# Optimization experiments

Hardware: AMD Instinct MI355X
Metric: run time of the kernel (lower is better)

The kernel has to match this reference:

```python
import jax, jax.numpy as jnp
import numpy as np

CHEB_K = 3


def setup_inputs() -> dict:
    key = jax.random.key(0)
    ks = jax.random.split(key, 7)
    B, N, D, E = 32, 2048, 64, 10
    return {
        "x": jax.random.normal(ks[0], (B, N, D), jnp.float32),
        "state": jnp.zeros((B, N, D), jnp.float32),
        "node_embeddings": jax.random.normal(ks[1], (N, E), jnp.float32),
        "gate_w_pool": 0.1 * jax.random.normal(ks[2], (E, CHEB_K, D, 2 * D), jnp.float32),
        "gate_b_pool": 0.1 * jax.random.normal(ks[3], (E, 2 * D), jnp.float32),
        "update_w_pool": 0.1 * jax.random.normal(ks[4], (E, CHEB_K, 2 * D, D), jnp.float32),
        "update_b_pool": 0.1 * jax.random.normal(ks[5], (E, D), jnp.float32),
    }


def _avwgcn(x, node_emb, w_pool, b_pool):
    # Adaptive adjacency from node embeddings: softmax(relu(E E^T)) over rows.
    N = node_emb.shape[0]
    adj = jax.nn.softmax(jax.nn.relu(node_emb @ node_emb.T), axis=1)  # [N,N]
    cheb = [jnp.eye(N, dtype=x.dtype), adj]
    for _ in range(2, CHEB_K):
        cheb.append(2.0 * adj @ cheb[-1] - cheb[-2])
    supports = jnp.stack(cheb, axis=0)  # [K,N,N]
    # Node-specific weights/bias from pools.
    weights = jnp.einsum('ne,ekio->nkio', node_emb, w_pool)  # [N,K,Ci,Co]
    bias = node_emb @ b_pool                                  # [N,Co]
    x_g = jnp.einsum('knm,bmi->bnki', supports, x)            # [B,N,K,Ci]
    return jnp.einsum('bnki,nkio->bno', x_g, weights) + bias  # [B,N,Co]


def reference(x, state, node_embeddings, gate_w_pool, gate_b_pool, update_w_pool, update_b_pool):
    # TGCRNCell.forward (note: `state` is ignored by the original forward;
    # input_and_state = x). dim_in == dim_out == hidden_dim.
    hidden_dim = x.shape[-1]
    z_r = jax.nn.sigmoid(_avwgcn(x, node_embeddings, gate_w_pool, gate_b_pool))
    z, r = z_r[..., :hidden_dim], z_r[..., hidden_dim:]
    candidate = jnp.concatenate([x, z], axis=-1)
    hc = jnp.tanh(_avwgcn(candidate, node_embeddings, update_w_pool, update_b_pool))
    h = r * x + (1.0 - r) * hc
    return h
```

## Files before the change

### kernel.cpp

```cpp
#include <hip/hip_runtime.h>

typedef _Float16 f16_t;
typedef float f32x4 __attribute__((ext_vector_type(4)));
typedef _Float16 f16x8 __attribute__((ext_vector_type(8)));

#define AS1 __attribute__((address_space(1)))
#define AS3 __attribute__((address_space(3)))

__device__ __forceinline__ void gload_lds16(const void* g, void* l) {
  __builtin_amdgcn_global_load_lds((const AS1 void*)g, (AS3 void*)l, 16, 0, 0);
}

__global__ __launch_bounds__(256) void adj_softmax(const float* __restrict__ emb,
                                                   f16_t* __restrict__ adjF) {
  __shared__ float vals[2048];
  __shared__ float red[16];
  const int n = blockIdx.x;
  const int t = threadIdx.x;
  const int lane = t & 63, wave = t >> 6;
  float en[10];
#pragma unroll
  for (int e = 0; e < 10; ++e) en[e] = emb[n * 10 + e];
  float lm = 0.0f;
  for (int m = t; m < 2048; m += 256) {
    const float* em = emb + m * 10;
    float d = 0.f;
#pragma unroll
    for (int e = 0; e < 10; ++e) d += en[e] * em[e];
    d = fmaxf(d, 0.0f);
    vals[m] = d;
    lm = fmaxf(lm, d);
  }
#pragma unroll
  for (int off = 32; off > 0; off >>= 1) lm = fmaxf(lm, __shfl_down(lm, off));
  if (lane == 0) red[wave] = lm;
  __syncthreads();
  const float gmax = fmaxf(fmaxf(red[0], red[1]), fmaxf(red[2], red[3]));
  float ls = 0.f;
  for (int m = t; m < 2048; m += 256) {
    float ev = expf(vals[m] - gmax);
    vals[m] = ev;
    ls += ev;
  }
#pragma unroll
  for (int off = 32; off > 0; off >>= 1) ls += __shfl_down(ls, off);
  if (lane == 0) red[8 + wave] = ls;
  __syncthreads();
  const float inv = 4096.0f / (red[8] + red[9] + red[10] + red[11]);
  for (int m = t; m < 2048; m += 256) {
    adjF[(long)n * 2048 + m] = (f16_t)(vals[m] * inv);
  }
}

__global__ __launch_bounds__(256) void split_xt(const float* __restrict__ x,
                                                f16_t* __restrict__ XTh) {
  __shared__ float tile[64][65];
  const int m0 = blockIdx.x * 64;
  const int b = blockIdx.y;
  const int tx = threadIdx.x & 63, ty = threadIdx.x >> 6;
  for (int r = ty; r < 64; r += 4)
    tile[r][tx] = x[(long)b * 131072 + (long)(m0 + r) * 64 + tx];
  __syncthreads();
  for (int r = ty; r < 64; r += 4) {
    long idx = (long)(b * 64 + r) * 2048 + m0 + tx;
    XTh[idx] = (f16_t)tile[tx][r];
  }
}

__global__ __launch_bounds__(256) void tsplit(const float* __restrict__ in,
                                              f16_t* __restrict__ oH, int R, int C) {
  __shared__ float tile[64][65];
  const int c0 = blockIdx.x * 64, r0 = blockIdx.y * 64;
  const int tx = threadIdx.x & 63, ty = threadIdx.x >> 6;
  for (int r = ty; r < 64; r += 4)
    tile[r][tx] = in[(long)(r0 + r) * C + c0 + tx];
  __syncthreads();
  for (int r = ty; r < 64; r += 4) {
    long idx = (long)(c0 + r) * R + r0 + tx;
    oH[idx] = (f16_t)tile[tx][r];
  }
}

__global__ __launch_bounds__(256) void permute_pool(const float* __restrict__ wp,
                                                    float* __restrict__ P,
                                                    int KI, int I, int O) {
  const int g = blockIdx.x * 256 + threadIdx.x;
  const int per = KI * O;
  const int e = g / per, rem = g % per;
  const int o = rem / KI, kk = rem % KI;
  const int k = kk / I, i = kk % I;
  P[g] = wp[(long)((e * 3 + k) * I + i) * O + o];
}

__global__ __launch_bounds__(256) void wgen(const float* __restrict__ P,
                                            const float* __restrict__ emb,
                                            f16_t* __restrict__ W) {
  __shared__ float es[160];
  const int c0 = blockIdx.x * 1024;
  const int n0 = blockIdx.y * 16;
  const int t = threadIdx.x;
  const int i4 = t * 4;
  if (t < 160) es[t] = emb[n0 * 10 + t];
  float4 p[10];
#pragma unroll
  for (int e = 0; e < 10; ++e)
    p[e] = *(const float4*)(P + (long)e * 24576 + c0 + i4);
  __syncthreads();
#pragma unroll 4
  for (int nn = 0; nn < 16; ++nn) {
    const float* ep = es + nn * 10;
    float v0 = 0.f, v1 = 0.f, v2 = 0.f, v3 = 0.f;
#pragma unroll
    for (int e = 0; e < 10; ++e) {
      const float ee = ep[e];
      v0 += ee * p[e].x; v1 += ee * p[e].y; v2 += ee * p[e].z; v3 += ee * p[e].w;
    }
    union { ushort4 u; f16_t h[4]; } o;
    o.h[0] = (f16_t)v0; o.h[1] = (f16_t)v1; o.h[2] = (f16_t)v2; o.h[3] = (f16_t)v3;
    *(ushort4*)(W + (long)(n0 + nn) * 24576 + c0 + i4) = o.u;
  }
}

template <int WT>
__global__ __launch_bounds__(256) void fgemm(const f16_t* __restrict__ A,
                                             const f16_t* __restrict__ B,
                                             float* __restrict__ Cf,
                                             f16_t* __restrict__ Th,
                                             int K, int ldc) {
  __shared__ __align__(16) f16_t Ash[128 * 64];
  __shared__ __align__(16) f16_t Bsh[64 * 64];
  const int t = threadIdx.x;
  const int wave = t >> 6, lane = t & 63;
  const long m0 = (long)blockIdx.y * 128;
  const long n0 = (long)blockIdx.x * 64;
  const int srow = t >> 3;
  const int sc8 = ((t & 7) ^ (srow & 7)) << 3;
  const int fr = lane & 15;
  const int quad = lane >> 4;
  const int wm = wave * 32;
  char* lA = (char*)Ash + wave * 1024;
  char* lB = (char*)Bsh + wave * 1024;
  f32x4 acc[2][4] = {};
  for (int k0 = 0; k0 < K; k0 += 64) {
#pragma unroll
    for (int q = 0; q < 4; ++q)
      gload_lds16(A + (m0 + q * 32 + srow) * K + k0 + sc8, lA + q * 4096);
#pragma unroll
    for (int q = 0; q < 2; ++q)
      gload_lds16(B + (n0 + q * 32 + srow) * K + k0 + sc8, lB + q * 4096);
    __syncthreads();
#pragma unroll
    for (int kh = 0; kh < 2; ++kh) {
      const int cbase = kh * 4 + quad;
      f16x8 ah[2], bh[4];
#pragma unroll
      for (int i = 0; i < 2; ++i) {
        const int r = wm + i * 16 + fr;
        ah[i] = *(const f16x8*)(Ash + r * 64 + ((cbase ^ (fr & 7)) << 3));
      }
#pragma unroll
      for (int j = 0; j < 4; ++j) {
        const int r = j * 16 + fr;
        bh[j] = *(const f16x8*)(Bsh + r * 64 + ((cbase ^ (fr & 7)) << 3));
      }
#pragma unroll
      for (int i = 0; i < 2; ++i)
#pragma unroll
        for (int j = 0; j < 4; ++j)
          acc[i][j] = __builtin_amdgcn_mfma_f32_16x16x32_f16(ah[i], bh[j], acc[i][j], 0, 0, 0);
    }
    __syncthreads();
  }
  const int crow = quad * 4, ccol = fr;
#pragma unroll
  for (int i = 0; i < 2; ++i)
#pragma unroll
    for (int j = 0; j < 4; ++j) {
      float v[4];
#pragma unroll
      for (int r = 0; r < 4; ++r) v[r] = acc[i][j][r] * 0.000244140625f;
      const long gmb = m0 + wm + i * 16 + crow;
      const long gn = n0 + j * 16 + ccol;
#pragma unroll
      for (int r = 0; r < 4; ++r) Cf[(gmb + r) * ldc + gn] = v[r];
      if (WT) {
        union { ushort4 u; f16_t h[4]; } ph;
#pragma unroll
        for (int r = 0; r < 4; ++r) ph.h[r] = (f16_t)v[r];
        *(ushort4*)(Th + gn * 2048 + gmb) = ph.u;
      }
    }
}

__global__ __launch_bounds__(256) void gate_kernel(
    const float* __restrict__ x, const float* __restrict__ Xg1f,
    const float* __restrict__ Xg2r, const f16_t* __restrict__ Wg,
    const float* __restrict__ bpool, const float* __restrict__ emb,
    float* __restrict__ Zf, f16_t* __restrict__ rb) {
  __shared__ __align__(16) f16_t Ahi[32 * 200];
  const int n = blockIdx.x;
  const int t = threadIdx.x;
  float en[10];
#pragma unroll
  for (int e = 0; e < 10; ++e) en[e] = emb[n * 10 + e];
  {
    const int b = t >> 3, i8 = (t & 7) * 8;
    const float* s0 = x + (long)b * 131072 + (long)n * 64 + i8;
    const float* s1 = Xg1f + (long)n * 2048 + b * 64 + i8;
    const float* s2 = Xg2r + (long)n * 2048 + b * 64 + i8;
    float v0[8], v1[8], v2[8];
#pragma unroll
    for (int j = 0; j < 8; ++j) v0[j] = s0[j];
#pragma unroll
    for (int j = 0; j < 8; ++j) v1[j] = s1[j];
#pragma unroll
    for (int j = 0; j < 8; ++j) v2[j] = 2.0f * s2[j] - v0[j];
    union { uint4 u; f16_t h[8]; } th;
#pragma unroll
    for (int j = 0; j < 8; ++j) th.h[j] = (f16_t)v0[j];
    *(uint4*)(Ahi + b * 200 + i8) = th.u;
#pragma unroll
    for (int j = 0; j < 8; ++j) th.h[j] = (f16_t)v1[j];
    *(uint4*)(Ahi + b * 200 + 64 + i8) = th.u;
#pragma unroll
    for (int j = 0; j < 8; ++j) th.h[j] = (f16_t)v2[j];
    *(uint4*)(Ahi + b * 200 + 128 + i8) = th.u;
  }
  __syncthreads();
  const int wave = t >> 6, lane = t & 63;
  const int ob = wave * 32;
  const int fr = lane & 15, qk = (lane >> 4) * 8;
  const f16_t* Wp0 = Wg + (long)n * 24576 + (ob + fr) * 192 + qk;
  const f16_t* Wp1 = Wp0 + 16 * 192;
  f32x4 acc[2][2] = {};
#pragma unroll
  for (int k0 = 0; k0 < 192; k0 += 32) {
    f16x8 b0 = *(const f16x8*)(Wp0 + k0);
    f16x8 b1 = *(const f16x8*)(Wp1 + k0);
    f16x8 a0 = *(const f16x8*)(Ahi + fr * 200 + k0 + qk);
    f16x8 a1 = *(const f16x8*)(Ahi + (16 + fr) * 200 + k0 + qk);
    acc[0][0] = __builtin_amdgcn_mfma_f32_16x16x32_f16(a0, b0, acc[0][0], 0, 0, 0);
    acc[1][0] = __builtin_amdgcn_mfma_f32_16x16x32_f16(a1, b0, acc[1][0], 0, 0, 0);
    acc[0][1] = __builtin_amdgcn_mfma_f32_16x16x32_f16(a0, b1, acc[0][1], 0, 0, 0);
    acc[1][1] = __builtin_amdgcn_mfma_f32_16x16x32_f16(a1, b1, acc[1][1], 0, 0, 0);
  }
  const int quad = lane >> 4;
#pragma unroll
  for (int j = 0; j < 2; ++j) {
    const int o = ob + j * 16 + fr;
    float bias = 0.f;
#pragma unroll
    for (int e = 0; e < 10; ++e) bias += en[e] * bpool[e * 128 + o];
#pragma unroll
    for (int i2 = 0; i2 < 2; ++i2)
#pragma unroll
      for (int r = 0; r < 4; ++r) {
        const int b = i2 * 16 + quad * 4 + r;
        float v = acc[i2][j][r] + bias;
        v = 1.0f / (1.0f + expf(-v));
        if (o < 64)
          Zf[(long)n * 2048 + b * 64 + o] = v;
        else
          rb[(long)n * 2048 + b * 64 + (o - 64)] = (f16_t)v;
      }
  }
}

__global__ __launch_bounds__(256) void update_kernel(
    const float* __restrict__ x, const float* __restrict__ Zf,
    const float* __restrict__ Xg1f, const float* __restrict__ Cgz1f,
    const float* __restrict__ Xg2r, const float* __restrict__ Cgz2r,
    const f16_t* __restrict__ Wu, const float* __restrict__ bpool,
    const float* __restrict__ emb, const f16_t* __restrict__ rb,
    float* __restrict__ out) {
  __shared__ __align__(16) f16_t Ahi[32 * 392];
  const int n = blockIdx.x;
  const int t = threadIdx.x;
  float en[10];
#pragma unroll
  for (int e = 0; e < 10; ++e) en[e] = emb[n * 10 + e];
#pragma unroll
  for (int r = 0; r < 2; ++r) {
    const int c = r * 2048 + t * 8;
    const int b = c >> 7, j = c & 127;
    const int lo64 = j & 63;
    const float* s0 = (j < 64) ? (x + (long)b * 131072 + (long)n * 64 + lo64)
                               : (Zf + (long)n * 2048 + b * 64 + lo64);
    const float* s1 = (j < 64) ? (Xg1f + (long)n * 2048 + b * 64 + lo64)
                               : (Cgz1f + (long)n * 2048 + b * 64 + lo64);
    const float* s2 = (j < 64) ? (Xg2r + (long)n * 2048 + b * 64 + lo64)
                               : (Cgz2r + (long)n * 2048 + b * 64 + lo64);
    float v0[8], v1[8], v2[8];
#pragma unroll
    for (int q = 0; q < 8; ++q) v0[q] = s0[q];
#pragma unroll
    for (int q = 0; q < 8; ++q) v1[q] = s1[q];
#pragma unroll
    for (int q = 0; q < 8; ++q) v2[q] = 2.0f * s2[q] - v0[q];
    union { uint4 u; f16_t h[8]; } th;
#pragma unroll
    for (int q = 0; q < 8; ++q) th.h[q] = (f16_t)v0[q];
    *(uint4*)(Ahi + b * 392 + j) = th.u;
#pragma unroll
    for (int q = 0; q < 8; ++q) th.h[q] = (f16_t)v1[q];
    *(uint4*)(Ahi + b * 392 + 128 + j) = th.u;
#pragma unroll
    for (int q = 0; q < 8; ++q) th.h[q] = (f16_t)v2[q];
    *(uint4*)(Ahi + b * 392 + 256 + j) = th.u;
  }
  __syncthreads();
  const int wave = t >> 6, lane = t & 63;
  const int ob = wave * 16;
  const int fr = lane & 15, qk = (lane >> 4) * 8;
  const f16_t* Wp = Wu + (long)n * 24576 + (ob + fr) * 384 + qk;
  f32x4 acc[2] = {};
#pragma unroll
  for (int k0 = 0; k0 < 384; k0 += 32) {
    f16x8 bhv = *(const f16x8*)(Wp + k0);
    f16x8 a0 = *(const f16x8*)(Ahi + fr * 392 + k0 + qk);
    f16x8 a1 = *(const f16x8*)(Ahi + (16 + fr) * 392 + k0 + qk);
    acc[0] = __builtin_amdgcn_mfma_f32_16x16x32_f16(a0, bhv, acc[0], 0, 0, 0);
    acc[1] = __builtin_amdgcn_mfma_f32_16x16x32_f16(a1, bhv, acc[1], 0, 0, 0);
  }
  const int quad = lane >> 4;
  const int og = ob + fr;
  float bias = 0.f;
#pragma unroll
  for (int e = 0; e < 10; ++e) bias += en[e] * bpool[e * 64 + og];
#pragma unroll
  for (int i2 = 0; i2 < 2; ++i2)
#pragma unroll
    for (int r = 0; r < 4; ++r) {
      const int b = i2 * 16 + quad * 4 + r;
      float hc = tanhf(acc[i2][r] + bias);
      float rr = (float)rb[(long)n * 2048 + b * 64 + og];
      float xv = x[(long)b * 131072 + (long)n * 64 + og];
      out[(long)b * 131072 + (long)n * 64 + og] = rr * xv + (1.0f - rr) * hc;
    }
}

extern "C" void kernel_launch(void* const* d_in, const int* in_sizes, int n_in,
                              void* d_out, int out_size, void* d_ws, size_t ws_size,
                              hipStream_t stream) {
  (void)in_sizes; (void)n_in; (void)out_size;
  const float* x   = (const float*)d_in[0];
  const float* emb = (const float*)d_in[2];
  const float* gwp = (const float*)d_in[3];
  const float* gbp = (const float*)d_in[4];
  const float* uwp = (const float*)d_in[5];
  const float* ubp = (const float*)d_in[6];
  float* out = (float*)d_out;
  char* ws = (char*)d_ws;

  if (ws_size < 194904064ull) return;

  float*  Xg1f  = (float*)(ws);
  float*  Xg2r  = (float*)(ws + 16777216);
  float*  Zf    = (float*)(ws + 33554432);
  f16_t*  T1h   = (f16_t*)(ws + 33554432);
  f16_t*  rb    = (f16_t*)(ws + 50331648);
  float*  Pg    = (float*)(ws + 58720256);
  float*  Pu    = (float*)(ws + 59703296);
  f16_t*  adjF  = (f16_t*)(ws + 60686336);
  f16_t*  Sh    = (f16_t*)(ws + 69074944);
  f16_t*  Wg    = (f16_t*)(ws + 85852160);
  f16_t*  T2h   = (f16_t*)(ws + 85852160);
  f16_t*  Wu    = (f16_t*)(ws + 60686336);
  float*  Cgz1f = (float*)(ws + 161349632);
  float*  Cgz2r = (float*)(ws + 178126848);

  permute_pool<<<960, 256, 0, stream>>>(gwp, Pg, 192, 64, 128);
  permute_pool<<<960, 256, 0, stream>>>(uwp, Pu, 384, 128, 64);
  wgen<<<dim3(24, 128), 256, 0, stream>>>(Pg, emb, Wg);
  adj_softmax<<<2048, 256, 0, stream>>>(emb, adjF);
  split_xt<<<dim3(32, 32), 256, 0, stream>>>(x, Sh);

  fgemm<1><<<dim3(32, 16), 256, 0, stream>>>(adjF, Sh, Xg1f, T1h, 2048, 2048);
  fgemm<0><<<dim3(32, 16), 256, 0, stream>>>(adjF, T1h, Xg2r, nullptr, 2048, 2048);

  gate_kernel<<<2048, 256, 0, stream>>>(x, Xg1f, Xg2r, Wg, gbp, emb, Zf, rb);

  tsplit<<<dim3(32, 32), 256, 0, stream>>>(Zf, Sh, 2048, 2048);
  fgemm<1><<<dim3(32, 16), 256, 0, stream>>>(adjF, Sh, Cgz1f, T2h, 2048, 2048);
  fgemm<0><<<dim3(32, 16), 256, 0, stream>>>(adjF, T2h, Cgz2r, nullptr, 2048, 2048);

  wgen<<<dim3(24, 128), 256, 0, stream>>>(Pu, emb, Wu);
  update_kernel<<<2048, 256, 0, stream>>>(x, Zf, Xg1f, Cgz1f, Xg2r, Cgz2r, Wu,
                                          ubp, emb, rb, out);
}
```

Measured before the change: 381.2 us.

## Store graph-conv intermediates in fp16 and widen weight generation stores

Intermediate buffers (Xg1, Xg2, Z, Cgz1, Cgz2) are written and read as fp16 instead of fp32. This halves memory traffic between the GEMMs, the gate/update kernels and tsplit, and shrinks the workspace layout to match. wgen now computes 8 outputs per thread and writes them with 128-bit nontemporal stores, so half as many blocks are launched. The risk is extra rounding error in the intermediates and the Chebyshev recombination.

```diff
diff --git a/kernel.cpp b/kernel.cpp
--- a/kernel.cpp
+++ b/kernel.cpp
@@ -3,6 +3,7 @@
 typedef _Float16 f16_t;
 typedef float f32x4 __attribute__((ext_vector_type(4)));
 typedef _Float16 f16x8 __attribute__((ext_vector_type(8)));
+typedef unsigned int u32x4 __attribute__((ext_vector_type(4)));
 
 #define AS1 __attribute__((address_space(1)))
 #define AS3 __attribute__((address_space(3)))
@@ -67,13 +68,13 @@
   }
 }
 
-__global__ __launch_bounds__(256) void tsplit(const float* __restrict__ in,
+__global__ __launch_bounds__(256) void tsplit(const f16_t* __restrict__ in,
                                               f16_t* __restrict__ oH, int R, int C) {
   __shared__ float tile[64][65];
   const int c0 = blockIdx.x * 64, r0 = blockIdx.y * 64;
   const int tx = threadIdx.x & 63, ty = threadIdx.x >> 6;
   for (int r = ty; r < 64; r += 4)
-    tile[r][tx] = in[(long)(r0 + r) * C + c0 + tx];
+    tile[r][tx] = (float)in[(long)(r0 + r) * C + c0 + tx];
   __syncthreads();
   for (int r = ty; r < 64; r += 4) {
     long idx = (long)(c0 + r) * R + r0 + tx;
@@ -96,35 +97,41 @@
                                             const float* __restrict__ emb,
                                             f16_t* __restrict__ W) {
   __shared__ float es[160];
-  const int c0 = blockIdx.x * 1024;
+  const int c0 = blockIdx.x * 2048;
   const int n0 = blockIdx.y * 16;
   const int t = threadIdx.x;
-  const int i4 = t * 4;
+  const int i8 = t * 8;
   if (t < 160) es[t] = emb[n0 * 10 + t];
-  float4 p[10];
-#pragma unroll
-  for (int e = 0; e < 10; ++e)
-    p[e] = *(const float4*)(P + (long)e * 24576 + c0 + i4);
-  __syncthreads();
-#pragma unroll 4
+  float4 pa[10], pb[10];
+#pragma unroll
+  for (int e = 0; e < 10; ++e) {
+    pa[e] = *(const float4*)(P + (long)e * 24576 + c0 + i8);
+    pb[e] = *(const float4*)(P + (long)e * 24576 + c0 + i8 + 4);
+  }
+  __syncthreads();
+#pragma unroll 2
   for (int nn = 0; nn < 16; ++nn) {
     const float* ep = es + nn * 10;
-    float v0 = 0.f, v1 = 0.f, v2 = 0.f, v3 = 0.f;
+    float v[8] = {0.f, 0.f, 0.f, 0.f, 0.f, 0.f, 0.f, 0.f};
 #pragma unroll
     for (int e = 0; e < 10; ++e) {
       const float ee = ep[e];
-      v0 += ee * p[e].x; v1 += ee * p[e].y; v2 += ee * p[e].z; v3 += ee * p[e].w;
-    }
-    union { ushort4 u; f16_t h[4]; } o;
-    o.h[0] = (f16_t)v0; o.h[1] = (f16_t)v1; o.h[2] = (f16_t)v2; o.h[3] = (f16_t)v3;
-    *(ushort4*)(W + (long)(n0 + nn) * 24576 + c0 + i4) = o.u;
+      v[0] += ee * pa[e].x; v[1] += ee * pa[e].y;
+      v[2] += ee * pa[e].z; v[3] += ee * pa[e].w;
+      v[4] += ee * pb[e].x; v[5] += ee * pb[e].y;
+      v[6] += ee * pb[e].z; v[7] += ee * pb[e].w;
+    }
+    union { u32x4 u; f16_t h[8]; } o;
+#pragma unroll
+    for (int q = 0; q < 8; ++q) o.h[q] = (f16_t)v[q];
+    __builtin_nontemporal_store(o.u, (u32x4*)(W + (long)(n0 + nn) * 24576 + c0 + i8));
   }
 }
 
 template <int WT>
 __global__ __launch_bounds__(256) void fgemm(const f16_t* __restrict__ A,
                                              const f16_t* __restrict__ B,
-                                             float* __restrict__ Cf,
+                                             f16_t* __restrict__ Ch,
                                              f16_t* __restrict__ Th,
                                              int K, int ldc) {
   __shared__ __align__(16) f16_t Ash[128 * 64];
@@ -176,27 +183,27 @@
   for (int i = 0; i < 2; ++i)
 #pragma unroll
     for (int j = 0; j < 4; ++j) {
-      float v[4];
-#pragma unroll
-      for (int r = 0; r < 4; ++r) v[r] = acc[i][j][r] * 0.000244140625f;
+      f16_t v[4];
+#pragma unroll
+      for (int r = 0; r < 4; ++r) v[r] = (f16_t)(acc[i][j][r] * 0.000244140625f);
       const long gmb = m0 + wm + i * 16 + crow;
       const long gn = n0 + j * 16 + ccol;
 #pragma unroll
-      for (int r = 0; r < 4; ++r) Cf[(gmb + r) * ldc + gn] = v[r];
+      for (int r = 0; r < 4; ++r) Ch[(gmb + r) * ldc + gn] = v[r];
       if (WT) {
         union { ushort4 u; f16_t h[4]; } ph;
 #pragma unroll
-        for (int r = 0; r < 4; ++r) ph.h[r] = (f16_t)v[r];
+        for (int r = 0; r < 4; ++r) ph.h[r] = v[r];
         *(ushort4*)(Th + gn * 2048 + gmb) = ph.u;
       }
     }
 }
 
 __global__ __launch_bounds__(256) void gate_kernel(
-    const float* __restrict__ x, const float* __restrict__ Xg1f,
-    const float* __restrict__ Xg2r, const f16_t* __restrict__ Wg,
+    const float* __restrict__ x, const f16_t* __restrict__ Xg1h,
+    const f16_t* __restrict__ Xg2h, const f16_t* __restrict__ Wg,
     const float* __restrict__ bpool, const float* __restrict__ emb,
-    float* __restrict__ Zf, f16_t* __restrict__ rb) {
+    f16_t* __restrict__ Zh, f16_t* __restrict__ rb) {
   __shared__ __align__(16) f16_t Ahi[32 * 200];
   const int n = blockIdx.x;
   const int t = threadIdx.x;
@@ -206,24 +213,20 @@
   {
     const int b = t >> 3, i8 = (t & 7) * 8;
     const float* s0 = x + (long)b * 131072 + (long)n * 64 + i8;
-    const float* s1 = Xg1f + (long)n * 2048 + b * 64 + i8;
-    const float* s2 = Xg2r + (long)n * 2048 + b * 64 + i8;
-    float v0[8], v1[8], v2[8];
+    f16x8 l1 = *(const f16x8*)(Xg1h + (long)n * 2048 + b * 64 + i8);
+    f16x8 l2 = *(const f16x8*)(Xg2h + (long)n * 2048 + b * 64 + i8);
+    float v0[8];
 #pragma unroll
     for (int j = 0; j < 8; ++j) v0[j] = s0[j];
-#pragma unroll
-    for (int j = 0; j < 8; ++j) v1[j] = s1[j];
-#pragma unroll
-    for (int j = 0; j < 8; ++j) v2[j] = 2.0f * s2[j] - v0[j];
     union { uint4 u; f16_t h[8]; } th;
 #pragma unroll
     for (int j = 0; j < 8; ++j) th.h[j] = (f16_t)v0[j];
     *(uint4*)(Ahi + b * 200 + i8) = th.u;
 #pragma unroll
-    for (int j = 0; j < 8; ++j) th.h[j] = (f16_t)v1[j];
+    for (int j = 0; j < 8; ++j) th.h[j] = l1[j];
     *(uint4*)(Ahi + b * 200 + 64 + i8) = th.u;
 #pragma unroll
-    for (int j = 0; j < 8; ++j) th.h[j] = (f16_t)v2[j];
+    for (int j = 0; j < 8; ++j) th.h[j] = (f16_t)(2.0f * (float)l2[j] - v0[j]);
     *(uint4*)(Ahi + b * 200 + 128 + i8) = th.u;
   }
   __syncthreads();
@@ -259,7 +262,7 @@
         float v = acc[i2][j][r] + bias;
         v = 1.0f / (1.0f + expf(-v));
         if (o < 64)
-          Zf[(long)n * 2048 + b * 64 + o] = v;
+          Zh[(long)n * 2048 + b * 64 + o] = (f16_t)v;
         else
           rb[(long)n * 2048 + b * 64 + (o - 64)] = (f16_t)v;
       }
@@ -267,9 +270,9 @@
 }
 
 __global__ __launch_bounds__(256) void update_kernel(
-    const float* __restrict__ x, const float* __restrict__ Zf,
-    const float* __restrict__ Xg1f, const float* __restrict__ Cgz1f,
-    const float* __restrict__ Xg2r, const float* __restrict__ Cgz2r,
+    const float* __restrict__ x, const f16_t* __restrict__ Zh,
+    const f16_t* __restrict__ Xg1h, const f16_t* __restrict__ Cgz1h,
+    const f16_t* __restrict__ Xg2h, const f16_t* __restrict__ Cgz2h,
     const f16_t* __restrict__ Wu, const float* __restrict__ bpool,
     const float* __restrict__ emb, const f16_t* __restrict__ rb,
     float* __restrict__ out) {
@@ -284,28 +287,31 @@
     const int c = r * 2048 + t * 8;
     const int b = c >> 7, j = c & 127;
     const int lo64 = j & 63;
-    const float* s0 = (j < 64) ? (x + (long)b * 131072 + (long)n * 64 + lo64)
-                               : (Zf + (long)n * 2048 + b * 64 + lo64);
-    const float* s1 = (j < 64) ? (Xg1f + (long)n * 2048 + b * 64 + lo64)
-                               : (Cgz1f + (long)n * 2048 + b * 64 + lo64);
-    const float* s2 = (j < 64) ? (Xg2r + (long)n * 2048 + b * 64 + lo64)
-                               : (Cgz2r + (long)n * 2048 + b * 64 + lo64);
-    float v0[8], v1[8], v2[8];
-#pragma unroll
-    for (int q = 0; q < 8; ++q) v0[q] = s0[q];
-#pragma unroll
-    for (int q = 0; q < 8; ++q) v1[q] = s1[q];
-#pragma unroll
-    for (int q = 0; q < 8; ++q) v2[q] = 2.0f * s2[q] - v0[q];
+    float v0[8];
+    if (j < 64) {
+      const float* s0 = x + (long)b * 131072 + (long)n * 64 + lo64;
+#pragma unroll
+      for (int q = 0; q < 8; ++q) v0[q] = s0[q];
+    } else {
+      f16x8 l0 = *(const f16x8*)(Zh + (long)n * 2048 + b * 64 + lo64);
+#pragma unroll
+      for (int q = 0; q < 8; ++q) v0[q] = (float)l0[q];
+    }
+    const f16_t* s1 = (j < 64) ? (Xg1h + (long)n * 2048 + b * 64 + lo64)
+                               : (Cgz1h + (long)n * 2048 + b * 64 + lo64);
+    const f16_t* s2 = (j < 64) ? (Xg2h + (long)n * 2048 + b * 64 + lo64)
+                               : (Cgz2h + (long)n * 2048 + b * 64 + lo64);
+    f16x8 l1 = *(const f16x8*)s1;
+    f16x8 l2 = *(const f16x8*)s2;
     union { uint4 u; f16_t h[8]; } th;
 #pragma unroll
     for (int q = 0; q < 8; ++q) th.h[q] = (f16_t)v0[q];
     *(uint4*)(Ahi + b * 392 + j) = th.u;
 #pragma unroll
-    for (int q = 0; q < 8; ++q) th.h[q] = (f16_t)v1[q];
+    for (int q = 0; q < 8; ++q) th.h[q] = l1[q];
     *(uint4*)(Ahi + b * 392 + 128 + j) = th.u;
 #pragma unroll
-    for (int q = 0; q < 8; ++q) th.h[q] = (f16_t)v2[q];
+    for (int q = 0; q < 8; ++q) th.h[q] = (f16_t)(2.0f * (float)l2[q] - v0[q]);
     *(uint4*)(Ahi + b * 392 + 256 + j) = th.u;
   }
   __syncthreads();
@@ -352,39 +358,39 @@
   float* out = (float*)d_out;
   char* ws = (char*)d_ws;
 
-  if (ws_size < 194904064ull) return;
-
-  float*  Xg1f  = (float*)(ws);
-  float*  Xg2r  = (float*)(ws + 16777216);
-  float*  Zf    = (float*)(ws + 33554432);
-  f16_t*  T1h   = (f16_t*)(ws + 33554432);
-  f16_t*  rb    = (f16_t*)(ws + 50331648);
-  float*  Pg    = (float*)(ws + 58720256);
-  float*  Pu    = (float*)(ws + 59703296);
-  f16_t*  adjF  = (f16_t*)(ws + 60686336);
-  f16_t*  Sh    = (f16_t*)(ws + 69074944);
-  f16_t*  Wg    = (f16_t*)(ws + 85852160);
-  f16_t*  T2h   = (f16_t*)(ws + 85852160);
-  f16_t*  Wu    = (f16_t*)(ws + 60686336);
-  float*  Cgz1f = (float*)(ws + 161349632);
-  float*  Cgz2r = (float*)(ws + 178126848);
+  if (ws_size < 169738240ull) return;
+
+  f16_t*  Xg1h  = (f16_t*)(ws);
+  f16_t*  Xg2h  = (f16_t*)(ws + 8388608);
+  f16_t*  Zh    = (f16_t*)(ws + 16777216);
+  f16_t*  T1h   = (f16_t*)(ws + 16777216);
+  f16_t*  rb    = (f16_t*)(ws + 25165824);
+  float*  Pg    = (float*)(ws + 33554432);
+  float*  Pu    = (float*)(ws + 34537472);
+  f16_t*  adjF  = (f16_t*)(ws + 35520512);
+  f16_t*  Sh    = (f16_t*)(ws + 43909120);
+  f16_t*  Wg    = (f16_t*)(ws + 52297728);
+  f16_t*  T2h   = (f16_t*)(ws + 52297728);
+  f16_t*  Wu    = (f16_t*)(ws + 52297728);
+  f16_t*  Cgz1h = (f16_t*)(ws + 152961024);
+  f16_t*  Cgz2h = (f16_t*)(ws + 161349632);
 
   permute_pool<<<960, 256, 0, stream>>>(gwp, Pg, 192, 64, 128);
   permute_pool<<<960, 256, 0, stream>>>(uwp, Pu, 384, 128, 64);
-  wgen<<<dim3(24, 128), 256, 0, stream>>>(Pg, emb, Wg);
+  wgen<<<dim3(12, 128), 256, 0, stream>>>(Pg, emb, Wg);
   adj_softmax<<<2048, 256, 0, stream>>>(emb, adjF);
   split_xt<<<dim3(32, 32), 256, 0, stream>>>(x, Sh);
 
-  fgemm<1><<<dim3(32, 16), 256, 0, stream>>>(adjF, Sh, Xg1f, T1h, 2048, 2048);
-  fgemm<0><<<dim3(32, 16), 256, 0, stream>>>(adjF, T1h, Xg2r, nullptr, 2048, 2048);
-
-  gate_kernel<<<2048, 256, 0, stream>>>(x, Xg1f, Xg2r, Wg, gbp, emb, Zf, rb);
-
-  tsplit<<<dim3(32, 32), 256, 0, stream>>>(Zf, Sh, 2048, 2048);
-  fgemm<1><<<dim3(32, 16), 256, 0, stream>>>(adjF, Sh, Cgz1f, T2h, 2048, 2048);
-  fgemm<0><<<dim3(32, 16), 256, 0, stream>>>(adjF, T2h, Cgz2r, nullptr, 2048, 2048);
-
-  wgen<<<dim3(24, 128), 256, 0, stream>>>(Pu, emb, Wu);
-  update_kernel<<<2048, 256, 0, stream>>>(x, Zf, Xg1f, Cgz1f, Xg2r, Cgz2r, Wu,
+  fgemm<1><<<dim3(32, 16), 256, 0, stream>>>(adjF, Sh, Xg1h, T1h, 2048, 2048);
+  fgemm<0><<<dim3(32, 16), 256, 0, stream>>>(adjF, T1h, Xg2h, nullptr, 2048, 2048);
+
+  gate_kernel<<<2048, 256, 0, stream>>>(x, Xg1h, Xg2h, Wg, gbp, emb, Zh, rb);
+
+  tsplit<<<dim3(32, 32), 256, 0, stream>>>(Zh, Sh, 2048, 2048);
+  fgemm<1><<<dim3(32, 16), 256, 0, stream>>>(adjF, Sh, Cgz1h, T2h, 2048, 2048);
+  fgemm<0><<<dim3(32, 16), 256, 0, stream>>>(adjF, T2h, Cgz2h, nullptr, 2048, 2048);
+
+  wgen<<<dim3(12, 128), 256, 0, stream>>>(Pu, emb, Wu);
+  update_kernel<<<2048, 256, 0, stream>>>(x, Zh, Xg1h, Cgz1h, Xg2h, Cgz2h, Wu,
                                           ubp, emb, rb, out);
 }
```

Measured after the change: 389.6 us. 1.02x slower.
